# Optimization experiments

Hardware: AMD Instinct MI355X
Metric: run time of the kernel (lower is better)

Reference implementation:

```python
import math
import jax, jax.numpy as jnp
import numpy as np

HEAD_NUM = 8
DIM = 512
D_K = DIM // HEAD_NUM  # 64
M_FEAT = 256
B, L = 4, 2048
STAB = 1e-5


def _orthogonal_gaussian(m, d, rng):
    num_squares = m // d
    blocks = []
    for _ in range(num_squares):
        q, _ = np.linalg.qr(rng.standard_normal((d, d)))
        blocks.append(q.T)
    rem = m - d * num_squares
    if rem:
        q, _ = np.linalg.qr(rng.standard_normal((d, d)))
        blocks.append(q.T[:rem])
    mat = np.concatenate(blocks, axis=0)
    mat = mat / math.sqrt(num_squares + rem / d)
    return mat.astype(np.float32)


def setup_inputs() -> dict:
    key = jax.random.key(0)
    ks = jax.random.split(key, 12)
    rng = np.random.default_rng(0)
    inp = {
        'query': jax.random.normal(ks[0], (B, L, DIM), jnp.float32),
        'key': jax.random.normal(ks[1], (B, L, DIM), jnp.float32),
        'value': jax.random.normal(ks[2], (B, L, DIM), jnp.float32),
        'proj': jnp.asarray(_orthogonal_gaussian(M_FEAT, D_K, rng)),  # [M, d_k]
        'w_q_w': jax.random.normal(ks[3], (DIM, DIM), jnp.float32) * 0.02,
        'w_q_b': jnp.zeros((DIM,), jnp.float32),
        'w_k_w': jax.random.normal(ks[4], (DIM, DIM), jnp.float32) * 0.02,
        'w_k_b': jnp.zeros((DIM,), jnp.float32),
        'w_v_w': jax.random.normal(ks[5], (DIM, DIM), jnp.float32) * 0.02,
        'w_v_b': jnp.zeros((DIM,), jnp.float32),
        'w_o_w': jax.random.normal(ks[6], (DIM, DIM), jnp.float32) * 0.02,
        'w_o_b': jnp.zeros((DIM,), jnp.float32),
    }
    return inp


def _relu_kernel(data, proj):
    # data: [B,L,H,D], proj: [M,D] -> [B,L,H,M]
    ratio = 1.0 / math.sqrt(proj.shape[0])
    return jax.nn.relu(ratio * jnp.einsum('blhd,md->blhm', data, proj)) + STAB


def _favor_causal(qp, kp, vs):
    # qp, kp: [L,B,H,M]; vs: [L,B,H,D] -> num [L,B,H,D], den [L,B,H]
    b, h, m = qp.shape[1], qp.shape[2], qp.shape[3]
    d = vs.shape[3]
    carry0 = (jnp.zeros((b, h, m, d), qp.dtype), jnp.zeros((b, h, m), qp.dtype))

    def step(carry, inp):
        s_kv, s_k = carry
        q_l, k_l, v_l = inp
        s_kv = s_kv + jnp.einsum('bhm,bhd->bhmd', k_l, v_l)
        s_k = s_k + k_l
        num = jnp.einsum('bhmd,bhm->bhd', s_kv, q_l)
        den = jnp.sum(q_l * s_k, axis=-1)
        return (s_kv, s_k), (num, den)

    _, (num, den) = jax.lax.scan(step, carry0, (qp, kp, vs))
    return num, den


def reference(query, key, value, proj, w_q_w, w_q_b, w_k_w, w_k_b, w_v_w, w_v_b, w_o_w, w_o_b):
    bsz = query.shape[0]
    q = (query @ w_q_w.T + w_q_b).reshape(bsz, -1, HEAD_NUM, D_K)
    k = (key @ w_k_w.T + w_k_b).reshape(bsz, -1, HEAD_NUM, D_K)
    v = (value @ w_v_w.T + w_v_b).reshape(bsz, -1, HEAD_NUM, D_K)
    qp = jnp.swapaxes(_relu_kernel(q, proj), 0, 1)  # [L,B,H,M]
    kp = jnp.swapaxes(_relu_kernel(k, proj), 0, 1)
    vs = jnp.swapaxes(v, 0, 1)                      # [L,B,H,D]
    num, den = _favor_causal(qp, kp, vs)
    attn = jnp.swapaxes(num, 0, 1) / jnp.swapaxes(den, 0, 1)[..., None]  # [B,L,H,D]
    attn = attn.reshape(bsz, -1, HEAD_NUM * D_K)
    return attn @ w_o_w.T + w_o_b
```

## Files before the change

### kernel.cpp

```cpp
#include <hip/hip_runtime.h>
#include <stdint.h>

#define B_ 4
#define L_ 2048
#define H_ 8
#define DK 64
#define M_ 256
#define DIM_ 512
#define NTOK (B_ * L_)
#define CHK 128
#define NC (L_ / CHK)
#define BH (B_ * H_)
#define RATIO 0.0625f
#define STABC 1e-5f

typedef unsigned short ushort_t;
typedef __attribute__((ext_vector_type(8))) short bf8v;
typedef __attribute__((ext_vector_type(4))) float f4v;

#define MFMA16(a, b, c) __builtin_amdgcn_mfma_f32_16x16x32_bf16(a, b, c, 0, 0, 0)

__device__ __forceinline__ ushort_t f2bf(float f) {
  uint32_t u = __float_as_uint(f);
  return (ushort_t)((u + 0x7fffu + ((u >> 16) & 1u)) >> 16);
}
__device__ __forceinline__ float bf2f(ushort_t u) { return __uint_as_float(((uint32_t)u) << 16); }

__device__ __forceinline__ void gll16(const void* g, void* l) {
  __builtin_amdgcn_global_load_lds((const __attribute__((address_space(1))) void*)g,
                                   (__attribute__((address_space(3))) void*)l, 16, 0, 0);
}

__device__ __forceinline__ bf8v ldfrag(const ushort_t* base, int row, int cb) {
  return *(const bf8v*)((const char*)base + row * 128 + (cb ^ ((row & 7) << 4)));
}
__device__ __forceinline__ bf8v ldfrag256(const ushort_t* base, int row, int cb) {
  return *(const bf8v*)((const char*)base + row * 256 + (cb ^ ((row & 7) << 4)));
}
__device__ __forceinline__ bf8v ldfrag512(const ushort_t* base, int row, int cb) {
  return *(const bf8v*)((const char*)base + row * 512 + (cb ^ ((row & 7) << 4)));
}

__global__ __launch_bounds__(256) void cvt_w(const float* __restrict__ wq, const float* __restrict__ wk,
                                             const float* __restrict__ wv, const float* __restrict__ wo,
                                             const float* __restrict__ pj, ushort_t* __restrict__ d) {
  int i = (blockIdx.x * 256 + threadIdx.x) * 8;
  const float* s;
  int off;
  if (i < 262144)       { s = wq; off = i; }
  else if (i < 524288)  { s = wk; off = i - 262144; }
  else if (i < 786432)  { s = wv; off = i - 524288; }
  else if (i < 1048576) { s = wo; off = i - 786432; }
  else                  { s = pj; off = i - 1048576; }
  float4 a = *(const float4*)(s + off);
  float4 b = *(const float4*)(s + off + 4);
  union { ushort_t u[8]; uint4 vv; } o;
  o.u[0] = f2bf(a.x); o.u[1] = f2bf(a.y); o.u[2] = f2bf(a.z); o.u[3] = f2bf(a.w);
  o.u[4] = f2bf(b.x); o.u[5] = f2bf(b.y); o.u[6] = f2bf(b.z); o.u[7] = f2bf(b.w);
  *(uint4*)(d + i) = o.vv;
}

__global__ __launch_bounds__(512) void qkvgemm_k(const float* __restrict__ q, const float* __restrict__ k,
                                                 const float* __restrict__ v, const ushort_t* __restrict__ Wc,
                                                 const float* __restrict__ bq, const float* __restrict__ bk,
                                                 const float* __restrict__ bv, ushort_t* __restrict__ XHq,
                                                 ushort_t* __restrict__ XHk, ushort_t* __restrict__ VT) {
  __shared__ char SB[49152];
  ushort_t* Tt = (ushort_t*)SB;
  const int z = blockIdx.z;
  const float* X = (z == 0) ? q : (z == 1) ? k : v;
  const ushort_t* Bw = Wc + (size_t)z * 262144;
  const float* bias = (z == 0) ? bq : (z == 1) ? bk : bv;
  const int tid = threadIdx.x, lane = tid & 63, w = tid >> 6;
  const int bm = blockIdx.x * 128, bn = blockIdx.y * 256;
  const int scol = (((lane & 7) * 16) ^ ((lane >> 3) << 4)) >> 1;
  const int fr = lane & 15, ks = lane >> 4, fq = lane >> 4;
  const int wr = (w >> 2) * 64, wc = (w & 3) * 64;
  f4v acc[4][4] = {};
  for (int t = 0; t < 8; ++t) {
    const int k0 = t * 64;
#pragma unroll
    for (int i = 0; i < 4; ++i)
      gll16(Bw + (size_t)(bn + w * 32 + i * 8 + (lane >> 3)) * DIM_ + k0 + scol,
            SB + 16384 + w * 4096 + i * 1024);
#pragma unroll
    for (int i = 0; i < 2; ++i) {
      int e = tid + i * 512;
      int r = e >> 3, g = e & 7;
      const float* src = X + (size_t)(bm + r) * DIM_ + k0 + g * 8;
      float4 f0 = *(const float4*)src;
      float4 f1 = *(const float4*)(src + 4);
      union { ushort_t u[8]; bf8v v8; } pk;
      pk.u[0] = f2bf(f0.x); pk.u[1] = f2bf(f0.y); pk.u[2] = f2bf(f0.z); pk.u[3] = f2bf(f0.w);
      pk.u[4] = f2bf(f1.x); pk.u[5] = f2bf(f1.y); pk.u[6] = f2bf(f1.z); pk.u[7] = f2bf(f1.w);
      *(bf8v*)(SB + r * 128 + ((g * 16) ^ ((r & 7) << 4))) = pk.v8;
    }
    __syncthreads();
#pragma unroll
    for (int kk = 0; kk < 2; ++kk) {
      const int cb = kk * 64 + ks * 16;
      bf8v av[4], bv2[4];
#pragma unroll
      for (int m = 0; m < 4; ++m) av[m] = ldfrag((const ushort_t*)SB, wr + m * 16 + fr, cb);
#pragma unroll
      for (int n = 0; n < 4; ++n) bv2[n] = ldfrag((const ushort_t*)(SB + 16384), wc + n * 16 + fr, cb);
#pragma unroll
      for (int m = 0; m < 4; ++m)
#pragma unroll
        for (int n = 0; n < 4; ++n) acc[m][n] = MFMA16(av[m], bv2[n], acc[m][n]);
    }
    __syncthreads();
  }
  if (z == 2) {
    for (int hh = 0; hh < 2; ++hh) {
      if (((w & 3) >> 1) == hh) {
        const int wcl = wc - hh * 128;
#pragma unroll
        for (int m = 0; m < 4; ++m)
#pragma unroll
          for (int n = 0; n < 4; ++n) {
            int cl = wcl + n * 16 + fr;
            float bsv = bias[bn + wc + n * 16 + fr];
#pragma unroll
            for (int j = 0; j < 4; ++j) {
              int rl = wr + m * 16 + fq * 4 + j;
              Tt[cl * 136 + rl] = f2bf(acc[m][n][j] + bsv);
            }
          }
      }
      __syncthreads();
      const int dl = tid >> 2, seg = tid & 3;
      const int c = bn + hh * 128 + dl;
      const int bh2 = (bm >> 11) * 8 + (c >> 6);
      const int drow = c & 63;
      size_t vbase = ((size_t)(bh2 * 64 + drow)) * L_ + (bm & 2047) + seg * 32;
#pragma unroll
      for (int qq = 0; qq < 4; ++qq)
        *(uint4*)&VT[vbase + qq * 8] = *(const uint4*)&Tt[dl * 136 + seg * 32 + qq * 8];
      __syncthreads();
    }
  } else {
    ushort_t* Y = (z == 0) ? XHq : XHk;
#pragma unroll
    for (int m = 0; m < 4; ++m)
#pragma unroll
      for (int n = 0; n < 4; ++n) {
        int col = bn + wc + n * 16 + fr;
        float bsv = bias[col];
#pragma unroll
        for (int j = 0; j < 4; ++j) {
          int row = bm + wr + m * 16 + fq * 4 + j;
          Y[(size_t)row * DIM_ + col] = f2bf(acc[m][n][j] + bsv);
        }
      }
  }
}

__global__ __launch_bounds__(256) void cp2_k(const ushort_t* __restrict__ XHk, const ushort_t* __restrict__ P,
                                             const ushort_t* __restrict__ VT, ushort_t* __restrict__ S) {
  __shared__ ushort_t Ps[256 * 64];
  __shared__ ushort_t Xs[128 * 64];
  __shared__ ushort_t Kt[256 * 128];
  const int ci = blockIdx.x, bh = blockIdx.y;
  const int b = bh >> 3, h = bh & 7;
  const int tid = threadIdx.x, lane = tid & 63, w = tid >> 6;
  const int srow = w * 8 + (lane >> 3);
  const int scol = (((lane & 7) * 16) ^ ((lane >> 3) << 4)) >> 1;
  const int fr = lane & 15, ks = lane >> 4, fq = lane >> 4;
  const int l0 = ci * CHK;
#pragma unroll
  for (int i = 0; i < 8; ++i)
    gll16(P + (size_t)(i * 32 + srow) * 64 + scol, (char*)Ps + i * 4096 + w * 1024);
#pragma unroll
  for (int i = 0; i < 4; ++i)
    gll16(XHk + (size_t)(b * L_ + l0 + i * 32 + srow) * DIM_ + h * 64 + scol, (char*)Xs + i * 4096 + w * 1024);
  __syncthreads();
  {
    f4v acc[4][8] = {};
#pragma unroll
    for (int kk = 0; kk < 2; ++kk) {
      const int cb = kk * 64 + ks * 16;
      bf8v av[4], bv[8];
#pragma unroll
      for (int m = 0; m < 4; ++m) av[m] = ldfrag(Ps, w * 64 + m * 16 + fr, cb);
#pragma unroll
      for (int n = 0; n < 8; ++n) bv[n] = ldfrag(Xs, n * 16 + fr, cb);
#pragma unroll
      for (int m = 0; m < 4; ++m)
#pragma unroll
        for (int n = 0; n < 8; ++n) acc[m][n] = MFMA16(av[m], bv[n], acc[m][n]);
    }
#pragma unroll
    for (int m = 0; m < 4; ++m)
#pragma unroll
      for (int n = 0; n < 8; ++n) {
        const int mb = w * 64 + m * 16 + fq * 4;
        const int ll = n * 16 + fr;
#pragma unroll
        for (int j = 0; j < 4; ++j) {
          float v = fmaxf(RATIO * acc[m][n][j], 0.f) + STABC;
          *(ushort_t*)((char*)Kt + (mb + j) * 256 + ((ll * 2) ^ (((mb + j) & 7) << 4))) = f2bf(v);
        }
      }
  }
  __syncthreads();
  f4v accS[5][4] = {};
  for (int kt = 0; kt < 2; ++kt) {
#pragma unroll
    for (int i = 0; i < 2; ++i)
      gll16(VT + ((size_t)bh * 64 + i * 32 + srow) * L_ + l0 + kt * 64 + scol, (char*)Xs + i * 4096 + w * 1024);
    if (tid < 32) ((uint32_t*)Xs)[2048 + tid] = 0x3f803f80u;
    __syncthreads();
#pragma unroll
    for (int kk = 0; kk < 2; ++kk) {
      const int cbA = kk * 64 + ks * 16;
      const int cbK = kt * 128 + kk * 64 + ks * 16;
      bf8v av[5], bv[4];
#pragma unroll
      for (int a = 0; a < 5; ++a) av[a] = ldfrag(Xs, a * 16 + fr, cbA);
#pragma unroll
      for (int n = 0; n < 4; ++n) bv[n] = ldfrag256(Kt, w * 64 + n * 16 + fr, cbK);
#pragma unroll
      for (int a = 0; a < 5; ++a)
#pragma unroll
        for (int n = 0; n < 4; ++n) accS[a][n] = MFMA16(av[a], bv[n], accS[a][n]);
    }
    __syncthreads();
  }
  const size_t base = ((size_t)bh * NC + ci) * 65;
#pragma unroll
  for (int a = 0; a < 5; ++a)
#pragma unroll
    for (int n = 0; n < 4; ++n)
#pragma unroll
      for (int j = 0; j < 4; ++j) {
        int row = a * 16 + fq * 4 + j;
        if (row < 65) S[(base + row) * M_ + w * 64 + n * 16 + fr] = f2bf(accS[a][n][j]);
      }
}

__global__ __launch_bounds__(256) void prefix2_k(ushort_t* __restrict__ S) {
  const int g = blockIdx.x * 256 + threadIdx.x;
  const int bh = g / 2080, r = g - bh * 2080;
  ushort_t* base = S + (size_t)bh * (NC * 65 * M_) + (size_t)r * 8;
  uint4 v[16];
#pragma unroll
  for (int ci = 0; ci < NC; ++ci) v[ci] = *(const uint4*)(base + (size_t)ci * (65 * M_));
  float c[8] = {};
#pragma unroll
  for (int ci = 0; ci < NC; ++ci) {
    union { uint4 u; ushort_t s[8]; } in, out;
    in.u = v[ci];
#pragma unroll
    for (int e = 0; e < 8; ++e) {
      float t = bf2f(in.s[e]);
      out.s[e] = f2bf(c[e]);
      c[e] += t;
    }
    *(uint4*)(base + (size_t)ci * (65 * M_)) = out.u;
  }
}

__global__ __launch_bounds__(512) void qkout4_k(const ushort_t* __restrict__ XHq, const ushort_t* __restrict__ XHk,
                                                const ushort_t* __restrict__ P, const ushort_t* __restrict__ VT,
                                                const ushort_t* __restrict__ S, ushort_t* __restrict__ attn) {
  __shared__ char LB[147456];
  ushort_t* Qp  = (ushort_t*)LB;
  ushort_t* Pj  = (ushort_t*)(LB + 65536);
  ushort_t* Kps = (ushort_t*)(LB + 98304);
  ushort_t* R2  = (ushort_t*)(LB + 114688);
  ushort_t* Xk  = (ushort_t*)(LB + 131072);
  const int ci = blockIdx.x, bh = blockIdx.y;
  const int b = bh >> 3, h = bh & 7;
  const int tid = threadIdx.x, lane = tid & 63, w = tid >> 6;
  const int srow = w * 8 + (lane >> 3);
  const int scol = (((lane & 7) * 16) ^ ((lane >> 3) << 4)) >> 1;
  const int fr = lane & 15, ks = lane >> 4, fq = lane >> 4;
  const int l0 = ci * CHK;
  const size_t tokb = (size_t)b * L_ + l0;
  const size_t sbase = ((size_t)bh * NC + ci) * 65;
#pragma unroll
  for (int i = 0; i < 4; ++i)
    gll16(P + (size_t)(i * 64 + srow) * 64 + scol, (char*)Pj + i * 8192 + w * 1024);
#pragma unroll
  for (int i = 0; i < 2; ++i) {
    gll16(XHq + (tokb + i * 64 + srow) * DIM_ + h * 64 + scol, (char*)R2 + i * 8192 + w * 1024);
    gll16(XHk + (tokb + i * 64 + srow) * DIM_ + h * 64 + scol, (char*)Xk + i * 8192 + w * 1024);
  }
  __syncthreads();
  {
    f4v accF[2][8] = {};
#pragma unroll
    for (int kk = 0; kk < 2; ++kk) {
      const int cb = kk * 64 + ks * 16;
      bf8v av[2], bv[8];
#pragma unroll
      for (int m = 0; m < 2; ++m) av[m] = ldfrag(Pj, w * 32 + m * 16 + fr, cb);
#pragma unroll
      for (int n = 0; n < 8; ++n) bv[n] = ldfrag(R2, n * 16 + fr, cb);
#pragma unroll
      for (int m = 0; m < 2; ++m)
#pragma unroll
        for (int n = 0; n < 8; ++n) accF[m][n] = MFMA16(av[m], bv[n], accF[m][n]);
    }
#pragma unroll
    for (int m = 0; m < 2; ++m)
#pragma unroll
      for (int n = 0; n < 8; ++n) {
        const int mb = w * 32 + m * 16 + fq * 4;
        const int ll = n * 16 + fr;
        ushort_t bvv[4];
#pragma unroll
        for (int j = 0; j < 4; ++j)
          bvv[j] = f2bf(fmaxf(RATIO * accF[m][n][j], 0.f) + STABC);
        uint2 pk;
        pk.x = (uint32_t)bvv[0] | ((uint32_t)bvv[1] << 16);
        pk.y = (uint32_t)bvv[2] | ((uint32_t)bvv[3] << 16);
        *(uint2*)((char*)Qp + ll * 512 + ((mb * 2) ^ ((ll & 7) << 4))) = pk;
      }
  }
  __syncthreads();
  const int qr = (w & 3) * 32, qc = (w >> 2) * 64;
  const int orow = w * 16;
  f4v accA[2][4] = {};
  f4v acc2[5] = {};
  for (int kt = 0; kt < 4; ++kt) {
    gll16(S + (sbase + srow) * M_ + kt * 64 + scol, (char*)R2 + w * 1024);
    if (tid < 32)
      ((uint32_t*)R2)[2048 + tid] = ((const uint32_t*)(S + (sbase + 64) * M_ + kt * 64))[tid];
    {
      const int fi = w >> 1, tf0 = (w & 1) * 4;
      f4v accK[4] = {};
#pragma unroll
      for (int kk = 0; kk < 2; ++kk) {
        const int cb = kk * 64 + ks * 16;
        bf8v ap = ldfrag(Pj, kt * 64 + fi * 16 + fr, cb);
        bf8v bx[4];
#pragma unroll
        for (int t2 = 0; t2 < 4; ++t2) bx[t2] = ldfrag(Xk, (tf0 + t2) * 16 + fr, cb);
#pragma unroll
        for (int t2 = 0; t2 < 4; ++t2) accK[t2] = MFMA16(ap, bx[t2], accK[t2]);
      }
#pragma unroll
      for (int t2 = 0; t2 < 4; ++t2) {
        const int tt = (tf0 + t2) * 16 + fr;
        const int fl = fi * 16 + fq * 4;
#pragma unroll
        for (int j = 0; j < 4; ++j) {
          float v = fmaxf(RATIO * accK[t2][j], 0.f) + STABC;
          *(ushort_t*)((char*)Kps + tt * 128 + (((fl + j) * 2) ^ ((tt & 7) << 4))) = f2bf(v);
        }
      }
    }
    __syncthreads();
#pragma unroll
    for (int kk = 0; kk < 2; ++kk) {
      const int cb = kk * 64 + ks * 16;
      const int cbQ = kt * 128 + cb;
      bf8v aq[2], bk_[4], a2, sv[5];
#pragma unroll
      for (int m = 0; m < 2; ++m) aq[m] = ldfrag512(Qp, qr + m * 16 + fr, cbQ);
#pragma unroll
      for (int n = 0; n < 4; ++n) bk_[n] = ldfrag(Kps, qc + n * 16 + fr, cb);
#pragma unroll
      for (int m = 0; m < 2; ++m)
#pragma unroll
        for (int n = 0; n < 4; ++n) accA[m][n] = MFMA16(aq[m], bk_[n], accA[m][n]);
      a2 = ldfrag512(Qp, orow + fr, cbQ);
#pragma unroll
      for (int n = 0; n < 5; ++n) sv[n] = ldfrag(R2, n * 16 + fr, cb);
#pragma unroll
      for (int n = 0; n < 5; ++n) acc2[n] = MFMA16(a2, sv[n], acc2[n]);
    }
    __syncthreads();
  }
#pragma unroll
  for (int m = 0; m < 2; ++m)
#pragma unroll
    for (int n = 0; n < 4; ++n)
#pragma unroll
      for (int j = 0; j < 4; ++j) {
        int row = qr + m * 16 + fq * 4 + j;
        int col = qc + n * 16 + fr;
        float v = (col <= row) ? accA[m][n][j] : 0.f;
        *(ushort_t*)((char*)Pj + row * 256 + ((col * 2) ^ ((row & 7) << 4))) = f2bf(v);
      }
  __syncthreads();
  for (int kt2 = 0; kt2 < 2; ++kt2) {
    gll16(VT + ((size_t)bh * 64 + srow) * L_ + l0 + kt2 * 64 + scol, (char*)R2 + w * 1024);
    if (tid < 32) ((uint32_t*)R2)[2048 + tid] = 0x3f803f80u;
    __syncthreads();
#pragma unroll
    for (int kk = 0; kk < 2; ++kk) {
      const int cb = kk * 64 + ks * 16;
      bf8v a3, sv[5];
      a3 = ldfrag256(Pj, orow + fr, kt2 * 128 + cb);
#pragma unroll
      for (int n = 0; n < 5; ++n) sv[n] = ldfrag(R2, n * 16 + fr, cb);
#pragma unroll
      for (int n = 0; n < 5; ++n) acc2[n] = MFMA16(a3, sv[n], acc2[n]);
    }
    __syncthreads();
  }
  float dinv[4];
#pragma unroll
  for (int j = 0; j < 4; ++j) {
    float den = __shfl(acc2[4][j], (lane & 48));
    dinv[j] = 1.f / den;
  }
#pragma unroll
  for (int n = 0; n < 4; ++n)
#pragma unroll
    for (int j = 0; j < 4; ++j) {
      int l = orow + fq * 4 + j;
      int col = h * 64 + n * 16 + fr;
      attn[(tokb + l) * DIM_ + col] = f2bf(acc2[n][j] * dinv[j]);
    }
}

__global__ __launch_bounds__(256) void gemmo_k(const ushort_t* __restrict__ A, const ushort_t* __restrict__ Bw,
                                               const float* __restrict__ bias, float* __restrict__ Y) {
  __shared__ char SB[49152];
  const int tid = threadIdx.x, lane = tid & 63, w = tid >> 6;
  const int bm = blockIdx.x * 128, bn = blockIdx.y * 64;
  const int srow = w * 8 + (lane >> 3);
  const int scol = (((lane & 7) * 16) ^ ((lane >> 3) << 4)) >> 1;
  const int wr = (w >> 1) * 64, wc = (w & 1) * 32;
  const int fr = lane & 15, ks = lane >> 4, fq = lane >> 4;
  f4v acc[4][2] = {};
#pragma unroll
  for (int i = 0; i < 4; ++i)
    gll16(A + (size_t)(bm + i * 32 + srow) * DIM_ + scol, SB + i * 4096 + w * 1024);
#pragma unroll
  for (int i = 0; i < 2; ++i)
    gll16(Bw + (size_t)(bn + i * 32 + srow) * DIM_ + scol, SB + 32768 + i * 4096 + w * 1024);
  __syncthreads();
  for (int t = 0; t < 8; ++t) {
    const ushort_t* curA = (const ushort_t*)(SB + (t & 1) * 16384);
    const ushort_t* curB = (const ushort_t*)(SB + 32768 + (t & 1) * 8192);
    char* nxtA = SB + ((t + 1) & 1) * 16384;
    char* nxtB = SB + 32768 + ((t + 1) & 1) * 8192;
    const int nk = (t + 1) * 64;
    if (t < 7) {
#pragma unroll
      for (int i = 0; i < 4; ++i)
        gll16(A + (size_t)(bm + i * 32 + srow) * DIM_ + nk + scol, nxtA + i * 4096 + w * 1024);
#pragma unroll
      for (int i = 0; i < 2; ++i)
        gll16(Bw + (size_t)(bn + i * 32 + srow) * DIM_ + nk + scol, nxtB + i * 4096 + w * 1024);
    }
#pragma unroll
    for (int kk = 0; kk < 2; ++kk) {
      const int cb = kk * 64 + ks * 16;
      bf8v av[4], bv[2];
#pragma unroll
      for (int m = 0; m < 4; ++m) av[m] = ldfrag(curA, wr + m * 16 + fr, cb);
#pragma unroll
      for (int n = 0; n < 2; ++n) bv[n] = ldfrag(curB, wc + n * 16 + fr, cb);
#pragma unroll
      for (int m = 0; m < 4; ++m)
#pragma unroll
        for (int n = 0; n < 2; ++n) acc[m][n] = MFMA16(av[m], bv[n], acc[m][n]);
    }
    __syncthreads();
  }
#pragma unroll
  for (int m = 0; m < 4; ++m)
#pragma unroll
    for (int n = 0; n < 2; ++n) {
      int col = bn + wc + n * 16 + fr;
      float bsv = bias[col];
#pragma unroll
      for (int j = 0; j < 4; ++j) {
        int row = bm + wr + m * 16 + fq * 4 + j;
        Y[(size_t)row * DIM_ + col] = acc[m][n][j] + bsv;
      }
    }
}

extern "C" void kernel_launch(void* const* d_in, const int* in_sizes, int n_in,
                              void* d_out, int out_size, void* d_ws, size_t ws_size,
                              hipStream_t stream) {
  const float* query = (const float*)d_in[0];
  const float* key   = (const float*)d_in[1];
  const float* value = (const float*)d_in[2];
  const float* proj  = (const float*)d_in[3];
  const float* wq = (const float*)d_in[4];
  const float* bq = (const float*)d_in[5];
  const float* wk = (const float*)d_in[6];
  const float* bk = (const float*)d_in[7];
  const float* wv = (const float*)d_in[8];
  const float* bv = (const float*)d_in[9];
  const float* wo = (const float*)d_in[10];
  const float* bo = (const float*)d_in[11];

  char* ws = (char*)d_ws;
  ushort_t* Wc   = (ushort_t*)(ws);
  ushort_t* XHq  = (ushort_t*)(ws + 2129920);
  ushort_t* XHk  = (ushort_t*)(ws + 10518528);
  ushort_t* VT   = (ushort_t*)(ws + 18907136);
  ushort_t* Skv  = (ushort_t*)(ws + 27295744);
  ushort_t* attb = (ushort_t*)(ws + 44335104);
  const ushort_t* Wo = Wc + 786432;
  const ushort_t* Pc = Wc + 1048576;

  dim3 blk(256);
  cvt_w<<<520, blk, 0, stream>>>(wq, wk, wv, wo, proj, Wc);
  qkvgemm_k<<<dim3(64, 2, 3), dim3(512), 0, stream>>>(query, key, value, Wc, bq, bk, bv, XHq, XHk, VT);
  cp2_k<<<dim3(NC, BH), blk, 0, stream>>>(XHk, Pc, VT, Skv);
  prefix2_k<<<260, blk, 0, stream>>>(Skv);
  qkout4_k<<<dim3(NC, BH), dim3(512), 0, stream>>>(XHq, XHk, Pc, VT, Skv, attb);
  gemmo_k<<<dim3(64, 8), blk, 0, stream>>>(attb, Wo, bo, (float*)d_out);
}
```

Baseline: 92.21 us.

## Pre-convert activations to bf16 and double-buffer QKV GEMM with async LDS loads

The fp32 query, key and value tensors are now converted to bf16 in one merged conversion kernel together with the weights, instead of being converted inside the QKV GEMM. The GEMM then streams both operands with global_load_lds into double-buffered shared memory, prefetching the next K slice while computing the current one. This is meant to overlap load latency with MFMA work and remove in-loop conversion. In exchange it adds a full extra bf16 write and read of the activations through global memory, and doubles LDS use to 96KB per block, which limits occupancy.

New measurement: 99.23 us. 7.6% more time.

```diff
diff --git a/kernel.cpp b/kernel.cpp
--- a/kernel.cpp
+++ b/kernel.cpp
@@ -41,69 +41,83 @@
   return *(const bf8v*)((const char*)base + row * 512 + (cb ^ ((row & 7) << 4)));
 }
 
-__global__ __launch_bounds__(256) void cvt_w(const float* __restrict__ wq, const float* __restrict__ wk,
-                                             const float* __restrict__ wv, const float* __restrict__ wo,
-                                             const float* __restrict__ pj, ushort_t* __restrict__ d) {
+__global__ __launch_bounds__(256) void cvt_all(const float* __restrict__ q, const float* __restrict__ k,
+                                               const float* __restrict__ v, const float* __restrict__ wq,
+                                               const float* __restrict__ wk, const float* __restrict__ wv,
+                                               const float* __restrict__ wo, const float* __restrict__ pj,
+                                               ushort_t* __restrict__ Xq, ushort_t* __restrict__ Xk,
+                                               ushort_t* __restrict__ Xv, ushort_t* __restrict__ Wc) {
   int i = (blockIdx.x * 256 + threadIdx.x) * 8;
   const float* s;
-  int off;
-  if (i < 262144)       { s = wq; off = i; }
-  else if (i < 524288)  { s = wk; off = i - 262144; }
-  else if (i < 786432)  { s = wv; off = i - 524288; }
-  else if (i < 1048576) { s = wo; off = i - 786432; }
-  else                  { s = pj; off = i - 1048576; }
-  float4 a = *(const float4*)(s + off);
-  float4 b = *(const float4*)(s + off + 4);
+  ushort_t* d;
+  int soff, doff;
+  if (i < 4194304)       { s = q;  d = Xq; soff = i;            doff = soff; }
+  else if (i < 8388608)  { s = k;  d = Xk; soff = i - 4194304;  doff = soff; }
+  else if (i < 12582912) { s = v;  d = Xv; soff = i - 8388608;  doff = soff; }
+  else {
+    int j = i - 12582912;
+    d = Wc; doff = j;
+    if (j < 262144)       { s = wq; soff = j; }
+    else if (j < 524288)  { s = wk; soff = j - 262144; }
+    else if (j < 786432)  { s = wv; soff = j - 524288; }
+    else if (j < 1048576) { s = wo; soff = j - 786432; }
+    else                  { s = pj; soff = j - 1048576; }
+  }
+  float4 a = *(const float4*)(s + soff);
+  float4 b = *(const float4*)(s + soff + 4);
   union { ushort_t u[8]; uint4 vv; } o;
   o.u[0] = f2bf(a.x); o.u[1] = f2bf(a.y); o.u[2] = f2bf(a.z); o.u[3] = f2bf(a.w);
   o.u[4] = f2bf(b.x); o.u[5] = f2bf(b.y); o.u[6] = f2bf(b.z); o.u[7] = f2bf(b.w);
-  *(uint4*)(d + i) = o.vv;
-}
-
-__global__ __launch_bounds__(512) void qkvgemm_k(const float* __restrict__ q, const float* __restrict__ k,
-                                                 const float* __restrict__ v, const ushort_t* __restrict__ Wc,
+  *(uint4*)(d + doff) = o.vv;
+}
+
+__global__ __launch_bounds__(512) void qkvgemm_k(const ushort_t* __restrict__ Xq, const ushort_t* __restrict__ Xk,
+                                                 const ushort_t* __restrict__ Xv, const ushort_t* __restrict__ Wc,
                                                  const float* __restrict__ bq, const float* __restrict__ bk,
                                                  const float* __restrict__ bv, ushort_t* __restrict__ XHq,
                                                  ushort_t* __restrict__ XHk, ushort_t* __restrict__ VT) {
-  __shared__ char SB[49152];
+  __shared__ char SB[98304];
   ushort_t* Tt = (ushort_t*)SB;
   const int z = blockIdx.z;
-  const float* X = (z == 0) ? q : (z == 1) ? k : v;
+  const ushort_t* A = (z == 0) ? Xq : (z == 1) ? Xk : Xv;
   const ushort_t* Bw = Wc + (size_t)z * 262144;
   const float* bias = (z == 0) ? bq : (z == 1) ? bk : bv;
   const int tid = threadIdx.x, lane = tid & 63, w = tid >> 6;
   const int bm = blockIdx.x * 128, bn = blockIdx.y * 256;
+  const int srow = w * 8 + (lane >> 3);
   const int scol = (((lane & 7) * 16) ^ ((lane >> 3) << 4)) >> 1;
   const int fr = lane & 15, ks = lane >> 4, fq = lane >> 4;
   const int wr = (w >> 2) * 64, wc = (w & 3) * 64;
   f4v acc[4][4] = {};
+#pragma unroll
+  for (int i = 0; i < 2; ++i)
+    gll16(A + (size_t)(bm + i * 64 + srow) * DIM_ + scol, SB + i * 8192 + w * 1024);
+#pragma unroll
+  for (int i = 0; i < 4; ++i)
+    gll16(Bw + (size_t)(bn + i * 64 + srow) * DIM_ + scol, SB + 32768 + i * 8192 + w * 1024);
+  __syncthreads();
   for (int t = 0; t < 8; ++t) {
-    const int k0 = t * 64;
-#pragma unroll
-    for (int i = 0; i < 4; ++i)
-      gll16(Bw + (size_t)(bn + w * 32 + i * 8 + (lane >> 3)) * DIM_ + k0 + scol,
-            SB + 16384 + w * 4096 + i * 1024);
-#pragma unroll
-    for (int i = 0; i < 2; ++i) {
-      int e = tid + i * 512;
-      int r = e >> 3, g = e & 7;
-      const float* src = X + (size_t)(bm + r) * DIM_ + k0 + g * 8;
-      float4 f0 = *(const float4*)src;
-      float4 f1 = *(const float4*)(src + 4);
-      union { ushort_t u[8]; bf8v v8; } pk;
-      pk.u[0] = f2bf(f0.x); pk.u[1] = f2bf(f0.y); pk.u[2] = f2bf(f0.z); pk.u[3] = f2bf(f0.w);
-      pk.u[4] = f2bf(f1.x); pk.u[5] = f2bf(f1.y); pk.u[6] = f2bf(f1.z); pk.u[7] = f2bf(f1.w);
-      *(bf8v*)(SB + r * 128 + ((g * 16) ^ ((r & 7) << 4))) = pk.v8;
-    }
-    __syncthreads();
+    const ushort_t* curA = (const ushort_t*)(SB + (t & 1) * 16384);
+    const ushort_t* curB = (const ushort_t*)(SB + 32768 + (t & 1) * 32768);
+    char* nxtA = SB + ((t + 1) & 1) * 16384;
+    char* nxtB = SB + 32768 + ((t + 1) & 1) * 32768;
+    const int nk = (t + 1) * 64;
+    if (t < 7) {
+#pragma unroll
+      for (int i = 0; i < 2; ++i)
+        gll16(A + (size_t)(bm + i * 64 + srow) * DIM_ + nk + scol, nxtA + i * 8192 + w * 1024);
+#pragma unroll
+      for (int i = 0; i < 4; ++i)
+        gll16(Bw + (size_t)(bn + i * 64 + srow) * DIM_ + nk + scol, nxtB + i * 8192 + w * 1024);
+    }
 #pragma unroll
     for (int kk = 0; kk < 2; ++kk) {
       const int cb = kk * 64 + ks * 16;
       bf8v av[4], bv2[4];
 #pragma unroll
-      for (int m = 0; m < 4; ++m) av[m] = ldfrag((const ushort_t*)SB, wr + m * 16 + fr, cb);
-#pragma unroll
-      for (int n = 0; n < 4; ++n) bv2[n] = ldfrag((const ushort_t*)(SB + 16384), wc + n * 16 + fr, cb);
+      for (int m = 0; m < 4; ++m) av[m] = ldfrag(curA, wr + m * 16 + fr, cb);
+#pragma unroll
+      for (int n = 0; n < 4; ++n) bv2[n] = ldfrag(curB, wc + n * 16 + fr, cb);
 #pragma unroll
       for (int m = 0; m < 4; ++m)
 #pragma unroll
@@ -496,17 +510,20 @@
 
   char* ws = (char*)d_ws;
   ushort_t* Wc   = (ushort_t*)(ws);
-  ushort_t* XHq  = (ushort_t*)(ws + 2129920);
-  ushort_t* XHk  = (ushort_t*)(ws + 10518528);
-  ushort_t* VT   = (ushort_t*)(ws + 18907136);
-  ushort_t* Skv  = (ushort_t*)(ws + 27295744);
-  ushort_t* attb = (ushort_t*)(ws + 44335104);
+  ushort_t* Xq   = (ushort_t*)(ws + 2129920);
+  ushort_t* Xk   = (ushort_t*)(ws + 10518528);
+  ushort_t* Xv   = (ushort_t*)(ws + 18907136);
+  ushort_t* XHq  = (ushort_t*)(ws + 27295744);
+  ushort_t* XHk  = (ushort_t*)(ws + 35684352);
+  ushort_t* VT   = (ushort_t*)(ws + 44072960);
+  ushort_t* Skv  = (ushort_t*)(ws + 52461568);
+  ushort_t* attb = (ushort_t*)(ws + 69500928);
   const ushort_t* Wo = Wc + 786432;
   const ushort_t* Pc = Wc + 1048576;
 
   dim3 blk(256);
-  cvt_w<<<520, blk, 0, stream>>>(wq, wk, wv, wo, proj, Wc);
-  qkvgemm_k<<<dim3(64, 2, 3), dim3(512), 0, stream>>>(query, key, value, Wc, bq, bk, bv, XHq, XHk, VT);
+  cvt_all<<<6664, blk, 0, stream>>>(query, key, value, wq, wk, wv, wo, proj, Xq, Xk, Xv, Wc);
+  qkvgemm_k<<<dim3(64, 2, 3), dim3(512), 0, stream>>>(Xq, Xk, Xv, Wc, bq, bk, bv, XHq, XHk, VT);
   cp2_k<<<dim3(NC, BH), blk, 0, stream>>>(XHk, Pc, VT, Skv);
   prefix2_k<<<260, blk, 0, stream>>>(Skv);
   qkout4_k<<<dim3(NC, BH), dim3(512), 0, stream>>>(XHq, XHk, Pc, VT, Skv, attb);
```
